# Optimization experiments

Measured on AMD Instinct MI355X. Metric: run time of the kernel, lower is better.

The kernel has to match this reference:

```python
import jax, jax.numpy as jnp
import numpy as np
import math

VOCAB = 256
EMBED = 1024
HEADS = 16
MAX_SEQ = 1024
B, S = 4, 1024
EPS = 1e-5


def setup_inputs() -> dict:
    key = jax.random.key(0)
    ks = jax.random.split(key, 10)
    x = jax.random.randint(ks[0], (B, S), 0, VOCAB)
    token_embedding = jax.random.normal(ks[1], (VOCAB, EMBED), dtype=jnp.float32)
    # positional phase buffer: pos * (1/10000**(dim/E)) * pi
    pos = jnp.arange(MAX_SEQ, dtype=jnp.float32)[:, None]
    dim = jnp.arange(EMBED, dtype=jnp.float32)[None, :]
    freq = 1.0 / (10000.0 ** (dim / EMBED))
    pos_phase = pos * freq * math.pi  # [MAX_SEQ, EMBED]
    hd = EMBED // HEADS
    q_rot = jax.random.uniform(ks[2], (HEADS, hd), minval=-math.pi, maxval=math.pi)
    k_rot = jax.random.uniform(ks[3], (HEADS, hd), minval=-math.pi, maxval=math.pi)
    v_rot = jax.random.uniform(ks[4], (HEADS, hd), minval=-math.pi, maxval=math.pi)
    # orthogonal-ish init for ff_real via QR
    a = jax.random.normal(ks[5], (EMBED, EMBED), dtype=jnp.float32)
    ff_real, _ = jnp.linalg.qr(a)
    ff_imag = jax.random.uniform(ks[6], (EMBED, EMBED), minval=-0.01, maxval=0.01)
    lim = 1.0 / math.sqrt(EMBED)
    ro_real_w = jax.random.uniform(ks[7], (VOCAB, EMBED), minval=-lim, maxval=lim)
    ro_real_b = jnp.zeros((VOCAB,), dtype=jnp.float32)
    ro_imag_w = jax.random.uniform(ks[8], (VOCAB, EMBED), minval=-lim, maxval=lim)
    ro_imag_b = jnp.zeros((VOCAB,), dtype=jnp.float32)
    return {
        "x": x,
        "token_embedding": token_embedding,
        "pos_phase": pos_phase,
        "q_rot": q_rot,
        "k_rot": k_rot,
        "v_rot": v_rot,
        "ff_real": ff_real,
        "ff_imag": ff_imag,
        "ro_real_w": ro_real_w,
        "ro_real_b": ro_real_b,
        "ro_imag_w": ro_imag_w,
        "ro_imag_b": ro_imag_b,
    }


def complex_norm(z):
    mag = jnp.abs(z)
    mean_mag = jnp.mean(mag, axis=-1, keepdims=True)
    std_mag = jnp.std(mag, axis=-1, keepdims=True, ddof=1)  # torch std is unbiased
    norm_mag = (mag - mean_mag) / (std_mag + EPS)
    scale = jnp.tanh(norm_mag) / (mag + EPS)
    return z * scale.astype(jnp.complex64)


def reference(x, token_embedding, pos_phase, q_rot, k_rot, v_rot,
              ff_real, ff_imag, ro_real_w, ro_real_b, ro_imag_w, ro_imag_b):
    b, s = x.shape
    h, hd = q_rot.shape
    mag = jnp.tanh(token_embedding[x])                       # [B,S,E]
    state = mag.astype(jnp.complex64) * jnp.exp(1j * pos_phase[:s].astype(jnp.complex64))[None]
    sh = state.reshape(b, s, h, hd)                          # [B,S,H,hd]
    q = sh * jnp.exp(1j * q_rot.astype(jnp.complex64))
    k = sh * jnp.exp(1j * k_rot.astype(jnp.complex64))
    v = sh * jnp.exp(1j * v_rot.astype(jnp.complex64))
    # complex QK^H interference -> take real part as logits
    interference = jnp.einsum('bqhd,bkhd->bhqk', q, jnp.conj(k))
    attn_logits = interference.real / math.sqrt(hd)
    causal = jnp.tril(jnp.ones((s, s), dtype=bool))
    attn_logits = jnp.where(causal[None, None], attn_logits, -jnp.inf)
    attn_weights = jax.nn.softmax(attn_logits * 8.0, axis=-1)  # [B,H,S,S]
    attn_out = jnp.einsum('bhqk,bkhd->bqhd', attn_weights.astype(jnp.complex64), v)
    attn_out = attn_out.reshape(b, s, h * hd)
    state = state + attn_out
    ff = ff_real.astype(jnp.complex64) + 1j * ff_imag.astype(jnp.complex64)
    state = state @ ff
    state = complex_norm(state)
    return state.real @ ro_real_w.T + ro_real_b + state.imag @ ro_imag_w.T + ro_imag_b
```

## Files before the change

kernel.cpp:

```cpp
#include <hip/hip_runtime.h>
#include <math.h>

#define B_ 4
#define S_ 1024
#define E_ 1024
#define H_ 16
#define V_ 256

typedef _Float16 h8 __attribute__((ext_vector_type(8)));
typedef _Float16 h4 __attribute__((ext_vector_type(4)));
typedef __fp16 f16x2 __attribute__((ext_vector_type(2)));
typedef int i2 __attribute__((ext_vector_type(2)));
typedef float f4x __attribute__((ext_vector_type(4)));

__device__ __forceinline__ void gload16(const void* g, void* l) {
  __builtin_amdgcn_global_load_lds((const __attribute__((address_space(1))) void*)g,
                                   (__attribute__((address_space(3))) void*)l, 16, 0, 0);
}

#define MFMA32F16(a, b, c) __builtin_amdgcn_mfma_f32_16x16x32_f16(a, b, c, 0, 0, 0)

#if defined(__has_builtin)
#if __has_builtin(__builtin_amdgcn_mfma_f32_16x16x16f16)
#define MFMA16F16(a, b, c) __builtin_amdgcn_mfma_f32_16x16x16f16(a, b, c, 0, 0, 0)
#endif
#endif
#ifndef MFMA16F16
__device__ __forceinline__ f4x mfma16f16_asm(h4 a, h4 b, f4x c) {
  asm volatile("v_mfma_f32_16x16x16_f16 %0, %1, %2, %0" : "+v"(c) : "v"(a), "v"(b));
  return c;
}
#define MFMA16F16(a, b, c) mfma16f16_asm(a, b, c)
#endif

__device__ __forceinline__ void fast_sincos(float x, float* s, float* c) {
  float rev = x * 0.15915494309189535f;
  rev = rev - floorf(rev);
  float sv, cv;
  asm("v_sin_f32 %0, %1" : "=v"(sv) : "v"(rev));
  asm("v_cos_f32 %0, %1" : "=v"(cv) : "v"(rev));
  *s = sv; *c = cv;
}
__device__ __forceinline__ float fast_tanh(float x) {
  return 1.0f - 2.0f / (__expf(2.0f * x) + 1.0f);
}
__device__ __forceinline__ float fast_exp2(float x) {
  float r;
  asm("v_exp_f32 %0, %1" : "=v"(r) : "v"(x));
  return r;
}

__global__ void rot_kernel(const float* __restrict__ qr, const float* __restrict__ kr,
                           const float* __restrict__ vr, float* __restrict__ tabs) {
  int i = blockIdx.x * blockDim.x + threadIdx.x;
  if (i >= 3 * 1024) return;
  int which = i >> 10;
  int j = i & 1023;
  const float* src = which == 0 ? qr : (which == 1 ? kr : vr);
  float s, c;
  sincosf(src[j], &s, &c);
  tabs[which * 2048 + j] = c;
  tabs[which * 2048 + 1024 + j] = s;
}

__global__ __launch_bounds__(256) void embed_qkv_kernel(
    const int* __restrict__ x, const float* __restrict__ te,
    const float* __restrict__ pp, const float* __restrict__ tabs,
    unsigned short* __restrict__ srh, unsigned short* __restrict__ sih,
    unsigned short* __restrict__ Kd, unsigned short* __restrict__ Vd) {
  __shared__ unsigned short Kl2[4096];
  __shared__ unsigned short Vl2[4096];
  const int kt2 = blockIdx.x;
  const int bh = blockIdx.y;
  const int b = bh >> 4, h = bh & 15;
  const int tid = threadIdx.x;
  const float* qc = tabs + h * 64;
  const float* qs = tabs + 1024 + h * 64;
  const float* kc = tabs + 2048 + h * 64;
  const float* ks = tabs + 3072 + h * 64;
  #pragma unroll
  for (int p = 0; p < 8; ++p) {
    int id = p * 256 + tid;
    int sl = id >> 6;
    int dd = id & 63;
    int s = kt2 * 32 + sl;
    int e = h * 64 + dd;
    int tok = x[b * 1024 + s];
    float mm = fast_tanh(te[tok * 1024 + e]);
    float sn, cs;
    fast_sincos(pp[s * 1024 + e], &sn, &cs);
    float re = mm * cs, im = mm * sn;
    size_t g = ((size_t)(b * 1024 + s)) * 1024 + e;
    *(_Float16*)&srh[g] = (_Float16)re;
    *(_Float16*)&sih[g] = (_Float16)im;
    float cq = qc[dd], sq = qs[dd], ck = kc[dd], sk = ks[dd];
    float cd = cq * ck + sq * sk;
    float sd = sq * ck - cq * sk;
    float kr = re * cd + im * sd;
    float ki = im * cd - re * sd;
    int t = sl >> 4, key = sl & 15;
    int c0 = dd, c1 = 64 + dd;
    #define KOFF(c) (t * 2048 + ((((c) >> 5) * 4 + (((c) >> 3) & 3)) * 16 + key) * 8 + ((c) & 7))
    *(_Float16*)&Kl2[KOFF(c0)] = (_Float16)kr;
    *(_Float16*)&Kl2[KOFF(c1)] = (_Float16)ki;
    #undef KOFF
    int kgk = key >> 2, jk = key & 3;
    #define VOFF(d) (t * 2048 + ((((d) >> 4) * 4 + kgk) * 16 + ((d) & 15)) * 4 + jk)
    *(_Float16*)&Vl2[VOFF(dd)] = (_Float16)re;
    *(_Float16*)&Vl2[VOFF(64 + dd)] = (_Float16)im;
    #undef VOFF
  }
  __syncthreads();
  unsigned short* kdst = Kd + ((size_t)(bh * 64 + kt2 * 2)) * 2048;
  unsigned short* vdst = Vd + ((size_t)(bh * 64 + kt2 * 2)) * 2048;
  #pragma unroll
  for (int p = 0; p < 2; ++p) {
    int c = p * 256 + tid;
    ((int4*)kdst)[c] = ((const int4*)Kl2)[c];
    ((int4*)vdst)[c] = ((const int4*)Vl2)[c];
  }
}

__global__ __launch_bounds__(256, 4) void attn_mfma_kernel(
    const unsigned short* __restrict__ srh, const unsigned short* __restrict__ sih,
    const unsigned short* __restrict__ Kd, const unsigned short* __restrict__ Vd,
    const float* __restrict__ tabs,
    unsigned short* __restrict__ Af) {
  __shared__ __align__(16) unsigned short Klds[2][4096];
  __shared__ __align__(16) unsigned short Vlds[2][4096];
  const int flat = blockIdx.x;
  const int low = flat & 7, rest = flat >> 3;
  const int a = rest >> 3;
  const int bh = ((rest & 7) << 3) | low;
  const int b = bh >> 4, h = bh & 15;
  const int tid = threadIdx.x, lane = tid & 63, wid = tid >> 6;
  const int cl = lane & 15, kg = lane >> 4;
  const int atile = (wid >> 1) ? (31 - a) : a;
  const int qw0 = atile * 32 + (wid & 1) * 16;

  h8 qf[4];
  {
    int q = qw0 + cl;
    const unsigned short* srow = srh + ((size_t)(b * 1024 + q)) * 1024 + h * 64;
    const unsigned short* irow = sih + ((size_t)(b * 1024 + q)) * 1024 + h * 64;
    #pragma unroll
    for (int ksx = 0; ksx < 4; ++ksx) {
      int f0 = ksx * 32 + kg * 8;
      qf[ksx] = (f0 < 64) ? *(const h8*)(srow + f0) : *(const h8*)(irow + (f0 - 64));
      qf[ksx] *= (_Float16)1.4426950408889634f;
    }
  }

  f4x acc[8] = {};
  float m_ = -1e30f, l_ = 0.f;
  const int np = 32 - a;
  const int wqmax = qw0 + 15;
  const int qcol = qw0 + cl;

  const unsigned short* kstream = Kd + ((size_t)(bh * 64)) * 2048;
  const unsigned short* vstream = Vd + ((size_t)(bh * 64)) * 2048;

  #define STAGE_PAIR(buf, P)                                                    \
    {                                                                           \
      const unsigned short* kb = kstream + (size_t)(P) * 4096;                  \
      const unsigned short* vb = vstream + (size_t)(P) * 4096;                  \
      _Pragma("unroll")                                                         \
      for (int r = 0; r < 2; ++r) {                                             \
        int off = r * 256 + wid * 64;                                           \
        gload16(kb + (size_t)(off + lane) * 8, &Klds[buf][off * 8]);            \
        gload16(vb + (size_t)(off + lane) * 8, &Vlds[buf][off * 8]);            \
      }                                                                         \
    }

  STAGE_PAIR(0, 0)
  __syncthreads();

  for (int p = 0; p < np; ++p) {
    const int cur = p & 1;
    if (p + 1 < np) STAGE_PAIR(cur ^ 1, p + 1)
    const int k0a = p * 32;
    if (k0a <= wqmax) {
      __builtin_amdgcn_s_setprio(1);
      f4x sca = {}, scb = {};
      #pragma unroll
      for (int ksx = 0; ksx < 4; ++ksx) {
        h8 ka = *(const h8*)&Klds[cur][ksx * 512 + lane * 8];
        sca = MFMA32F16(ka, qf[ksx], sca);
      }
      #pragma unroll
      for (int ksx = 0; ksx < 4; ++ksx) {
        h8 kb = *(const h8*)&Klds[cur][2048 + ksx * 512 + lane * 8];
        scb = MFMA32F16(kb, qf[ksx], scb);
      }
      __builtin_amdgcn_s_setprio(0);
      if (k0a + 31 > qw0) {
        #pragma unroll
        for (int r = 0; r < 4; ++r) {
          if (k0a + kg * 4 + r > qcol)      sca[r] = -1e30f;
          if (k0a + 16 + kg * 4 + r > qcol) scb[r] = -1e30f;
        }
      }
      float mA = fmaxf(fmaxf(sca[0], sca[1]), sca[2]);
      float mB = fmaxf(fmaxf(sca[3], scb[0]), scb[1]);
      float mC = fmaxf(fmaxf(scb[2], scb[3]), mA);
      float mx = fmaxf(mB, mC);
      mx = fmaxf(mx, __shfl_xor(mx, 16, 64));
      mx = fmaxf(mx, __shfl_xor(mx, 32, 64));
      if (!__all(mx <= m_ + 11.5416f)) {
        float mn = fmaxf(m_, mx);
        float corr = fast_exp2(m_ - mn);
        #pragma unroll
        for (int mt = 0; mt < 8; ++mt) acc[mt] *= corr;
        l_ *= corr;
        m_ = mn;
      }
      float pa0 = fast_exp2(sca[0] - m_), pa1 = fast_exp2(sca[1] - m_);
      float pa2 = fast_exp2(sca[2] - m_), pa3 = fast_exp2(sca[3] - m_);
      float pb0 = fast_exp2(scb[0] - m_), pb1 = fast_exp2(scb[1] - m_);
      float pb2 = fast_exp2(scb[2] - m_), pb3 = fast_exp2(scb[3] - m_);
      l_ += ((pa0 + pa1) + (pa2 + pa3)) + ((pb0 + pb1) + (pb2 + pb3));
      f16x2 a01 = __builtin_amdgcn_cvt_pkrtz(pa0, pa1);
      f16x2 a23 = __builtin_amdgcn_cvt_pkrtz(pa2, pa3);
      f16x2 b01 = __builtin_amdgcn_cvt_pkrtz(pb0, pb1);
      f16x2 b23 = __builtin_amdgcn_cvt_pkrtz(pb2, pb3);
      i2 ta, tb;
      ta[0] = __builtin_bit_cast(int, a01); ta[1] = __builtin_bit_cast(int, a23);
      tb[0] = __builtin_bit_cast(int, b01); tb[1] = __builtin_bit_cast(int, b23);
      h4 pba = __builtin_bit_cast(h4, ta);
      h4 pbb = __builtin_bit_cast(h4, tb);
      __builtin_amdgcn_s_setprio(1);
      #pragma unroll
      for (int mt = 0; mt < 8; ++mt) {
        h4 va = *(const h4*)&Vlds[cur][mt * 256 + lane * 4];
        acc[mt] = MFMA16F16(va, pba, acc[mt]);
      }
      #pragma unroll
      for (int mt = 0; mt < 8; ++mt) {
        h4 vb = *(const h4*)&Vlds[cur][2048 + mt * 256 + lane * 4];
        acc[mt] = MFMA16F16(vb, pbb, acc[mt]);
      }
      __builtin_amdgcn_s_setprio(0);
    }
    __syncthreads();
  }
  #undef STAGE_PAIR
  {
    l_ += __shfl_xor(l_, 16, 64);
    l_ += __shfl_xor(l_, 32, 64);
    float linv = 1.0f / l_;
    int q = qw0 + cl;
    size_t mrow = (size_t)(b * 1024 + q);
    size_t obase = mrow * 1024 + h * 64;
    size_t abase = mrow * 2048 + h * 64;
    #pragma unroll
    for (int mt = 0; mt < 4; ++mt) {
      int d0 = mt * 16 + kg * 4;
      h4 s_r = *(const h4*)&srh[obase + d0];
      h4 s_i = *(const h4*)&sih[obase + d0];
      h4 hr, hi;
      #pragma unroll
      for (int r = 0; r < 4; ++r) {
        int d = d0 + r;
        float orv = acc[mt][r] * linv;
        float oiv = acc[mt + 4][r] * linv;
        float c = tabs[4096 + h * 64 + d], s = tabs[5120 + h * 64 + d];
        hr[r] = (_Float16)(orv * c - oiv * s + (float)s_r[r]);
        hi[r] = (_Float16)(orv * s + oiv * c + (float)s_i[r]);
      }
      *(h4*)&Af[abase + d0]        = hr;
      *(h4*)&Af[abase + 1024 + d0] = hi;
    }
  }
}

__global__ void split_b_kernel(const float* __restrict__ fr, const float* __restrict__ fi,
                               unsigned short* __restrict__ Bt) {
  __shared__ float tile[32][33];
  const int k0 = blockIdx.x * 32, n0 = blockIdx.y * 32;
  const int tid = threadIdx.x;
  #pragma unroll
  for (int p = 0; p < 4; ++p) {
    int e = p * 256 + tid;
    int kk = e >> 5, nn = e & 31;
    int k = k0 + kk, n = n0 + nn;
    float v;
    if (n < 1024) v = (k < 1024) ? fr[(size_t)k * 1024 + n] : -fi[(size_t)(k - 1024) * 1024 + n];
    else          v = (k < 1024) ? fi[(size_t)k * 1024 + (n - 1024)]
                                 : fr[(size_t)(k - 1024) * 1024 + (n - 1024)];
    tile[kk][nn] = v;
  }
  __syncthreads();
  #pragma unroll
  for (int p = 0; p < 4; ++p) {
    int e = p * 256 + tid;
    int nn = e >> 5, kk = e & 31;
    *(_Float16*)&Bt[(size_t)(n0 + nn) * 2048 + (k0 + kk)] = (_Float16)tile[kk][nn];
  }
}

__global__ void split_w_kernel(const float* __restrict__ wr, const float* __restrict__ wi,
                               unsigned short* __restrict__ Wt) {
  int idx = blockIdx.x * 256 + threadIdx.x;
  int v = idx >> 9;
  int k4 = (idx & 511) * 4;
  float4 a = (k4 < 1024) ? *(const float4*)&wr[(size_t)v * 1024 + k4]
                         : *(const float4*)&wi[(size_t)v * 1024 + k4 - 1024];
  h4 h;
  h[0] = (_Float16)a.x; h[1] = (_Float16)a.y;
  h[2] = (_Float16)a.z; h[3] = (_Float16)a.w;
  *(h4*)&Wt[(size_t)v * 2048 + k4] = h;
}

__global__ __launch_bounds__(256, 4) void gemm_ff(
    const unsigned short* __restrict__ A,
    const unsigned short* __restrict__ Bt,
    float* __restrict__ pr0, float* __restrict__ pi0,
    float* __restrict__ pr1, float* __restrict__ pi1) {
  __shared__ short As[128 * 64];
  __shared__ short Bs[128 * 64];
  const int tid = threadIdx.x;
  const int lane = tid & 63, wid = tid >> 6;
  const int l = blockIdx.x + (blockIdx.y << 5);
  const int xcd = l & 7, j = l >> 3;
  const int m0 = ((xcd << 2) + (j & 3)) << 7;
  const int n0 = (j >> 2) << 7;
  const int z = blockIdx.z;
  const int wr = wid >> 1, wc = wid & 1;
  const int cl = lane & 15, rg = lane >> 4;

  f4x acc[4][4] = {};
  const int cbase = wid * 256;

  for (int kt = z * 16; kt < z * 16 + 16; ++kt) {
    const int k0 = kt * 64;
    #pragma unroll
    for (int it = 0; it < 4; ++it) {
      int c = cbase + it * 64 + lane;
      gload16(A + (size_t)(m0 + (c >> 3)) * 2048 + k0 + (c & 7) * 8,
              As + (cbase + it * 64) * 8);
      gload16(Bt + (size_t)(n0 + (c >> 3)) * 2048 + k0 + (c & 7) * 8,
              Bs + (cbase + it * 64) * 8);
    }
    __syncthreads();
    #pragma unroll
    for (int ks = 0; ks < 2; ++ks) {
      h8 a[4], b[4];
      #pragma unroll
      for (int ms = 0; ms < 4; ++ms)
        a[ms] = *(const h8*)&As[(wr * 64 + ms * 16 + cl) * 64 + ks * 32 + rg * 8];
      #pragma unroll
      for (int ns = 0; ns < 4; ++ns)
        b[ns] = *(const h8*)&Bs[(wc * 64 + ns * 16 + cl) * 64 + ks * 32 + rg * 8];
      #pragma unroll
      for (int ms = 0; ms < 4; ++ms)
        #pragma unroll
        for (int ns = 0; ns < 4; ++ns)
          acc[ms][ns] = MFMA32F16(a[ms], b[ns], acc[ms][ns]);
    }
    __syncthreads();
  }

  const int colbase = n0 + wc * 64;
  float* o_r = z ? pr1 : pr0;
  float* o_i = z ? pi1 : pi0;
  float* dst = (colbase < 1024) ? o_r : o_i;
  const int cb = colbase & 1023;
  #pragma unroll
  for (int ms = 0; ms < 4; ++ms)
    #pragma unroll
    for (int r2 = 0; r2 < 4; ++r2) {
      const int grow = m0 + wr * 64 + ms * 16 + rg * 4 + r2;
      #pragma unroll
      for (int ns = 0; ns < 4; ++ns)
        dst[(size_t)grow * 1024 + cb + ns * 16 + cl] = acc[ms][ns][r2];
    }
}

__global__ __launch_bounds__(256, 4) void gemm_ro(
    const unsigned short* __restrict__ Z,
    const unsigned short* __restrict__ Wt,
    float* __restrict__ part) {
  __shared__ short As[128 * 64];
  __shared__ short Bs[128 * 64];
  const int tid = threadIdx.x;
  const int lane = tid & 63, wid = tid >> 6;
  const int l = blockIdx.x + (blockIdx.y << 5);
  const int xcd = l & 7, j = l >> 3;
  const int m0 = ((xcd << 2) + (j & 3)) << 7;
  const int n0 = (j >> 2) << 7;
  const int z = blockIdx.z;
  const int wr = wid >> 1, wc = wid & 1;
  const int cl = lane & 15, rg = lane >> 4;

  f4x acc[4][4] = {};
  const int cbase = wid * 256;

  for (int kt = z * 8; kt < z * 8 + 8; ++kt) {
    const int k0 = kt * 64;
    #pragma unroll
    for (int it = 0; it < 4; ++it) {
      int c = cbase + it * 64 + lane;
      gload16(Z + (size_t)(m0 + (c >> 3)) * 2048 + k0 + (c & 7) * 8,
              As + (cbase + it * 64) * 8);
      gload16(Wt + (size_t)(n0 + (c >> 3)) * 2048 + k0 + (c & 7) * 8,
              Bs + (cbase + it * 64) * 8);
    }
    __syncthreads();
    #pragma unroll
    for (int ks = 0; ks < 2; ++ks) {
      h8 a[4], b[4];
      #pragma unroll
      for (int ms = 0; ms < 4; ++ms)
        a[ms] = *(const h8*)&As[(wr * 64 + ms * 16 + cl) * 64 + ks * 32 + rg * 8];
      #pragma unroll
      for (int ns = 0; ns < 4; ++ns)
        b[ns] = *(const h8*)&Bs[(wc * 64 + ns * 16 + cl) * 64 + ks * 32 + rg * 8];
      #pragma unroll
      for (int ms = 0; ms < 4; ++ms)
        #pragma unroll
        for (int ns = 0; ns < 4; ++ns)
          acc[ms][ns] = MFMA32F16(a[ms], b[ns], acc[ms][ns]);
    }
    __syncthreads();
  }

  float* dst = part + (size_t)z * 4096 * 256;
  const int colbase = n0 + wc * 64;
  #pragma unroll
  for (int ms = 0; ms < 4; ++ms)
    #pragma unroll
    for (int r2 = 0; r2 < 4; ++r2) {
      const int grow = m0 + wr * 64 + ms * 16 + rg * 4 + r2;
      #pragma unroll
      for (int ns = 0; ns < 4; ++ns)
        dst[(size_t)grow * 256 + colbase + ns * 16 + cl] = acc[ms][ns][r2];
    }
}

__global__ __launch_bounds__(256) void norm_split_kernel(
    const float* __restrict__ pr0, const float* __restrict__ pi0,
    const float* __restrict__ pr1, const float* __restrict__ pi1,
    unsigned short* __restrict__ Z) {
  const int row = blockIdx.x, tid = threadIdx.x;
  const int base = row * E_ + tid * 4;
  float4 r0 = *(const float4*)&pr0[base];
  float4 r1 = *(const float4*)&pr1[base];
  float4 i0 = *(const float4*)&pi0[base];
  float4 i1 = *(const float4*)&pi1[base];
  float4 zr = make_float4(r0.x + r1.x, r0.y + r1.y, r0.z + r1.z, r0.w + r1.w);
  float4 zi = make_float4(i0.x + i1.x, i0.y + i1.y, i0.z + i1.z, i0.w + i1.w);
  float mg[4];
  mg[0] = sqrtf(zr.x * zr.x + zi.x * zi.x);
  mg[1] = sqrtf(zr.y * zr.y + zi.y * zi.y);
  mg[2] = sqrtf(zr.z * zr.z + zi.z * zi.z);
  mg[3] = sqrtf(zr.w * zr.w + zi.w * zi.w);
  float s1 = mg[0] + mg[1] + mg[2] + mg[3];
  float s2 = mg[0]*mg[0] + mg[1]*mg[1] + mg[2]*mg[2] + mg[3]*mg[3];
  #pragma unroll
  for (int off = 1; off < 64; off <<= 1) {
    s1 += __shfl_xor(s1, off, 64);
    s2 += __shfl_xor(s2, off, 64);
  }
  __shared__ float ws1[4], ws2[4];
  if ((tid & 63) == 0) { ws1[tid >> 6] = s1; ws2[tid >> 6] = s2; }
  __syncthreads();
  s1 = ws1[0] + ws1[1] + ws1[2] + ws1[3];
  s2 = ws2[0] + ws2[1] + ws2[2] + ws2[3];
  float mean = s1 * (1.0f / 1024.0f);
  float var = (s2 - 1024.0f * mean * mean) * (1.0f / 1023.0f);
  var = fmaxf(var, 0.0f);
  float inv_sd = 1.0f / (sqrtf(var) + 1e-5f);
  float sc[4];
  #pragma unroll
  for (int t = 0; t < 4; ++t)
    sc[t] = tanhf((mg[t] - mean) * inv_sd) / (mg[t] + 1e-5f);
  h4 hr, hi;
  hr[0] = (_Float16)(zr.x * sc[0]); hr[1] = (_Float16)(zr.y * sc[1]);
  hr[2] = (_Float16)(zr.z * sc[2]); hr[3] = (_Float16)(zr.w * sc[3]);
  hi[0] = (_Float16)(zi.x * sc[0]); hi[1] = (_Float16)(zi.y * sc[1]);
  hi[2] = (_Float16)(zi.z * sc[2]); hi[3] = (_Float16)(zi.w * sc[3]);
  const size_t zb = (size_t)row * 2048 + tid * 4;
  *(h4*)&Z[zb]        = hr;
  *(h4*)&Z[zb + 1024] = hi;
}

__global__ void reduce_bias_kernel(const float* __restrict__ part,
                                   const float* __restrict__ rb,
                                   const float* __restrict__ ib,
                                   float* __restrict__ out) {
  int i4 = (blockIdx.x * 256 + threadIdx.x) * 4;
  int col = i4 & 255;
  float4 s = *(const float4*)&part[i4];
  #pragma unroll
  for (int z = 1; z < 4; ++z) {
    float4 v = *(const float4*)&part[(size_t)z * 1048576 + i4];
    s.x += v.x; s.y += v.y; s.z += v.z; s.w += v.w;
  }
  s.x += rb[col + 0] + ib[col + 0];
  s.y += rb[col + 1] + ib[col + 1];
  s.z += rb[col + 2] + ib[col + 2];
  s.w += rb[col + 3] + ib[col + 3];
  *(float4*)&out[i4] = s;
}

extern "C" void kernel_launch(void* const* d_in, const int* in_sizes, int n_in,
                              void* d_out, int out_size, void* d_ws, size_t ws_size,
                              hipStream_t stream) {
  const int*   x    = (const int*)d_in[0];
  const float* te   = (const float*)d_in[1];
  const float* pp   = (const float*)d_in[2];
  const float* qr   = (const float*)d_in[3];
  const float* kr   = (const float*)d_in[4];
  const float* vr   = (const float*)d_in[5];
  const float* ffr  = (const float*)d_in[6];
  const float* ffi  = (const float*)d_in[7];
  const float* rorw = (const float*)d_in[8];
  const float* rorb = (const float*)d_in[9];
  const float* roiw = (const float*)d_in[10];
  const float* roib = (const float*)d_in[11];
  float* out = (float*)d_out;

  char* W = (char*)d_ws;
  const size_t MiB = 1 << 20;
  unsigned short* srh = (unsigned short*)W;
  unsigned short* sih = (unsigned short*)(W + 16 * MiB);
  unsigned short* Af = (unsigned short*)(W + 32 * MiB);
  unsigned short* Kd = (unsigned short*)(W + 48 * MiB);
  unsigned short* Vd = (unsigned short*)(W + 64 * MiB);
  unsigned short* Bt = (unsigned short*)(W + 48 * MiB);
  unsigned short* Wt = (unsigned short*)(W + 56 * MiB);
  float* tabs = (float*)(W + 96 * MiB);
  float* pr0 = (float*)W;
  float* pi0 = (float*)(W + 16 * MiB);
  float* pr1 = (float*)(W + 64 * MiB);
  float* pi1 = (float*)(W + 80 * MiB);
  unsigned short* Zhl = Af;
  float* ro_part = (float*)(W + 64 * MiB);

  rot_kernel<<<12, 256, 0, stream>>>(qr, kr, vr, tabs);
  embed_qkv_kernel<<<dim3(32, 64), 256, 0, stream>>>(x, te, pp, tabs, srh, sih, Kd, Vd);
  attn_mfma_kernel<<<1024, 256, 0, stream>>>(srh, sih, Kd, Vd, tabs, Af);
  split_b_kernel<<<dim3(64, 64), 256, 0, stream>>>(ffr, ffi, Bt);
  split_w_kernel<<<512, 256, 0, stream>>>(rorw, roiw, Wt);
  gemm_ff<<<dim3(32, 16, 2), 256, 0, stream>>>(Af, Bt, pr0, pi0, pr1, pi1);
  norm_split_kernel<<<B_ * S_, 256, 0, stream>>>(pr0, pi0, pr1, pi1, Zhl);
  gemm_ro<<<dim3(32, 2, 4), 256, 0, stream>>>(Zhl, Wt, ro_part);
  reduce_bias_kernel<<<1024, 256, 0, stream>>>(ro_part, rorb, roib, out);
}
```

Measured before the change: 145.9 us.

## Double-buffer LDS tiles in feed-forward and readout GEMMs

Both MFMA GEMM kernels now keep two LDS stages for the A and B tiles. The first two K-tiles are prefetched up front, and the load for tile t+2 is issued right after the barrier that ends compute on tile t. This lets global-to-LDS copies overlap the MFMA work on the next tile instead of serialising load, barrier and compute. In exchange LDS per block doubles and launch bounds drop from 4 to 2 blocks per CU, so there is less latency hiding from occupancy.

```diff
diff --git a/kernel.cpp b/kernel.cpp
--- a/kernel.cpp
+++ b/kernel.cpp
@@ -311,13 +311,13 @@
   *(h4*)&Wt[(size_t)v * 2048 + k4] = h;
 }
 
-__global__ __launch_bounds__(256, 4) void gemm_ff(
+__global__ __launch_bounds__(256, 2) void gemm_ff(
     const unsigned short* __restrict__ A,
     const unsigned short* __restrict__ Bt,
     float* __restrict__ pr0, float* __restrict__ pi0,
     float* __restrict__ pr1, float* __restrict__ pi1) {
-  __shared__ short As[128 * 64];
-  __shared__ short Bs[128 * 64];
+  __shared__ short As[2][128 * 64];
+  __shared__ short Bs[2][128 * 64];
   const int tid = threadIdx.x;
   const int lane = tid & 63, wid = tid >> 6;
   const int l = blockIdx.x + (blockIdx.y << 5);
@@ -327,30 +327,39 @@
   const int z = blockIdx.z;
   const int wr = wid >> 1, wc = wid & 1;
   const int cl = lane & 15, rg = lane >> 4;
+  const int cbase = wid * 256;
 
   f4x acc[4][4] = {};
-  const int cbase = wid * 256;
-
-  for (int kt = z * 16; kt < z * 16 + 16; ++kt) {
-    const int k0 = kt * 64;
-    #pragma unroll
-    for (int it = 0; it < 4; ++it) {
-      int c = cbase + it * 64 + lane;
-      gload16(A + (size_t)(m0 + (c >> 3)) * 2048 + k0 + (c & 7) * 8,
-              As + (cbase + it * 64) * 8);
-      gload16(Bt + (size_t)(n0 + (c >> 3)) * 2048 + k0 + (c & 7) * 8,
-              Bs + (cbase + it * 64) * 8);
-    }
-    __syncthreads();
+
+  #define FF_STAGE(bf, kt)                                                      \
+    {                                                                           \
+      const int k0s = (kt) * 64;                                                \
+      _Pragma("unroll")                                                         \
+      for (int it = 0; it < 4; ++it) {                                          \
+        int c = cbase + it * 64 + lane;                                         \
+        gload16(A + (size_t)(m0 + (c >> 3)) * 2048 + k0s + (c & 7) * 8,         \
+                As[bf] + (cbase + it * 64) * 8);                                \
+        gload16(Bt + (size_t)(n0 + (c >> 3)) * 2048 + k0s + (c & 7) * 8,        \
+                Bs[bf] + (cbase + it * 64) * 8);                                \
+      }                                                                         \
+    }
+
+  const int ktbase = z * 16;
+  FF_STAGE(0, ktbase)
+  FF_STAGE(1, ktbase + 1)
+  __syncthreads();
+
+  for (int t = 0; t < 16; ++t) {
+    const int bf = t & 1;
     #pragma unroll
     for (int ks = 0; ks < 2; ++ks) {
       h8 a[4], b[4];
       #pragma unroll
       for (int ms = 0; ms < 4; ++ms)
-        a[ms] = *(const h8*)&As[(wr * 64 + ms * 16 + cl) * 64 + ks * 32 + rg * 8];
+        a[ms] = *(const h8*)&As[bf][(wr * 64 + ms * 16 + cl) * 64 + ks * 32 + rg * 8];
       #pragma unroll
       for (int ns = 0; ns < 4; ++ns)
-        b[ns] = *(const h8*)&Bs[(wc * 64 + ns * 16 + cl) * 64 + ks * 32 + rg * 8];
+        b[ns] = *(const h8*)&Bs[bf][(wc * 64 + ns * 16 + cl) * 64 + ks * 32 + rg * 8];
       #pragma unroll
       for (int ms = 0; ms < 4; ++ms)
         #pragma unroll
@@ -358,7 +367,9 @@
           acc[ms][ns] = MFMA32F16(a[ms], b[ns], acc[ms][ns]);
     }
     __syncthreads();
-  }
+    if (t + 2 < 16) FF_STAGE(bf, ktbase + t + 2)
+  }
+  #undef FF_STAGE
 
   const int colbase = n0 + wc * 64;
   float* o_r = z ? pr1 : pr0;
@@ -376,12 +387,12 @@
     }
 }
 
-__global__ __launch_bounds__(256, 4) void gemm_ro(
+__global__ __launch_bounds__(256, 2) void gemm_ro(
     const unsigned short* __restrict__ Z,
     const unsigned short* __restrict__ Wt,
     float* __restrict__ part) {
-  __shared__ short As[128 * 64];
-  __shared__ short Bs[128 * 64];
+  __shared__ short As[2][128 * 64];
+  __shared__ short Bs[2][128 * 64];
   const int tid = threadIdx.x;
   const int lane = tid & 63, wid = tid >> 6;
   const int l = blockIdx.x + (blockIdx.y << 5);
@@ -391,30 +402,39 @@
   const int z = blockIdx.z;
   const int wr = wid >> 1, wc = wid & 1;
   const int cl = lane & 15, rg = lane >> 4;
+  const int cbase = wid * 256;
 
   f4x acc[4][4] = {};
-  const int cbase = wid * 256;
-
-  for (int kt = z * 8; kt < z * 8 + 8; ++kt) {
-    const int k0 = kt * 64;
-    #pragma unroll
-    for (int it = 0; it < 4; ++it) {
-      int c = cbase + it * 64 + lane;
-      gload16(Z + (size_t)(m0 + (c >> 3)) * 2048 + k0 + (c & 7) * 8,
-              As + (cbase + it * 64) * 8);
-      gload16(Wt + (size_t)(n0 + (c >> 3)) * 2048 + k0 + (c & 7) * 8,
-              Bs + (cbase + it * 64) * 8);
-    }
-    __syncthreads();
+
+  #define RO_STAGE(bf, kt)                                                      \
+    {                                                                           \
+      const int k0s = (kt) * 64;                                                \
+      _Pragma("unroll")                                                         \
+      for (int it = 0; it < 4; ++it) {                                          \
+        int c = cbase + it * 64 + lane;                                         \
+        gload16(Z + (size_t)(m0 + (c >> 3)) * 2048 + k0s + (c & 7) * 8,         \
+                As[bf] + (cbase + it * 64) * 8);                                \
+        gload16(Wt + (size_t)(n0 + (c >> 3)) * 2048 + k0s + (c & 7) * 8,        \
+                Bs[bf] + (cbase + it * 64) * 8);                                \
+      }                                                                         \
+    }
+
+  const int ktbase = z * 8;
+  RO_STAGE(0, ktbase)
+  RO_STAGE(1, ktbase + 1)
+  __syncthreads();
+
+  for (int t = 0; t < 8; ++t) {
+    const int bf = t & 1;
     #pragma unroll
     for (int ks = 0; ks < 2; ++ks) {
       h8 a[4], b[4];
       #pragma unroll
       for (int ms = 0; ms < 4; ++ms)
-        a[ms] = *(const h8*)&As[(wr * 64 + ms * 16 + cl) * 64 + ks * 32 + rg * 8];
+        a[ms] = *(const h8*)&As[bf][(wr * 64 + ms * 16 + cl) * 64 + ks * 32 + rg * 8];
       #pragma unroll
       for (int ns = 0; ns < 4; ++ns)
-        b[ns] = *(const h8*)&Bs[(wc * 64 + ns * 16 + cl) * 64 + ks * 32 + rg * 8];
+        b[ns] = *(const h8*)&Bs[bf][(wc * 64 + ns * 16 + cl) * 64 + ks * 32 + rg * 8];
       #pragma unroll
       for (int ms = 0; ms < 4; ++ms)
         #pragma unroll
@@ -422,7 +442,9 @@
           acc[ms][ns] = MFMA32F16(a[ms], b[ns], acc[ms][ns]);
     }
     __syncthreads();
-  }
+    if (t + 2 < 8) RO_STAGE(bf, ktbase + t + 2)
+  }
+  #undef RO_STAGE
 
   float* dst = part + (size_t)z * 4096 * 256;
   const int colbase = n0 + wc * 64;
```

Measured after the change: 156.5 us. +7.2%, slower.

## Double-buffer LDS tiles in gemm_ff with a K-step of 32

Applied to the files above, without the earlier changes.

The single 128x64 LDS tile per operand in gemm_ff becomes two 128x32 buffers. Loads for step t+2 are issued right after the barrier that ends compute on step t, so global-to-LDS transfers overlap with MFMA work on the other buffer. Total LDS use stays the same, but the K-step is halved, so there are twice as many barriers per block. Any overlap also depends on how the barrier's waitcnt handling interacts with the in-flight global_load_lds.

```diff
diff --git a/kernel.cpp b/kernel.cpp
--- a/kernel.cpp
+++ b/kernel.cpp
@@ -316,8 +316,8 @@
     const unsigned short* __restrict__ Bt,
     float* __restrict__ pr0, float* __restrict__ pi0,
     float* __restrict__ pr1, float* __restrict__ pi1) {
-  __shared__ short As[128 * 64];
-  __shared__ short Bs[128 * 64];
+  __shared__ short As[2][128 * 32];
+  __shared__ short Bs[2][128 * 32];
   const int tid = threadIdx.x;
   const int lane = tid & 63, wid = tid >> 6;
   const int l = blockIdx.x + (blockIdx.y << 5);
@@ -327,38 +327,46 @@
   const int z = blockIdx.z;
   const int wr = wid >> 1, wc = wid & 1;
   const int cl = lane & 15, rg = lane >> 4;
+  const int cb2 = wid * 128;
 
   f4x acc[4][4] = {};
-  const int cbase = wid * 256;
-
-  for (int kt = z * 16; kt < z * 16 + 16; ++kt) {
-    const int k0 = kt * 64;
-    #pragma unroll
-    for (int it = 0; it < 4; ++it) {
-      int c = cbase + it * 64 + lane;
-      gload16(A + (size_t)(m0 + (c >> 3)) * 2048 + k0 + (c & 7) * 8,
-              As + (cbase + it * 64) * 8);
-      gload16(Bt + (size_t)(n0 + (c >> 3)) * 2048 + k0 + (c & 7) * 8,
-              Bs + (cbase + it * 64) * 8);
-    }
+
+  #define FF_STAGE(bf, kt)                                                      \
+    {                                                                           \
+      const int k0s = (kt) * 32;                                                \
+      _Pragma("unroll")                                                         \
+      for (int it = 0; it < 2; ++it) {                                          \
+        int c = cb2 + it * 64 + lane;                                           \
+        gload16(A + (size_t)(m0 + (c >> 2)) * 2048 + k0s + (c & 3) * 8,         \
+                As[bf] + (cb2 + it * 64) * 8);                                  \
+        gload16(Bt + (size_t)(n0 + (c >> 2)) * 2048 + k0s + (c & 3) * 8,        \
+                Bs[bf] + (cb2 + it * 64) * 8);                                  \
+      }                                                                         \
+    }
+
+  const int ktbase = z * 32;
+  FF_STAGE(0, ktbase)
+  FF_STAGE(1, ktbase + 1)
+  __syncthreads();
+
+  for (int t = 0; t < 32; ++t) {
+    const int bf = t & 1;
+    h8 a[4], b[4];
+    #pragma unroll
+    for (int ms = 0; ms < 4; ++ms)
+      a[ms] = *(const h8*)&As[bf][(wr * 64 + ms * 16 + cl) * 32 + rg * 8];
+    #pragma unroll
+    for (int ns = 0; ns < 4; ++ns)
+      b[ns] = *(const h8*)&Bs[bf][(wc * 64 + ns * 16 + cl) * 32 + rg * 8];
+    #pragma unroll
+    for (int ms = 0; ms < 4; ++ms)
+      #pragma unroll
+      for (int ns = 0; ns < 4; ++ns)
+        acc[ms][ns] = MFMA32F16(a[ms], b[ns], acc[ms][ns]);
     __syncthreads();
-    #pragma unroll
-    for (int ks = 0; ks < 2; ++ks) {
-      h8 a[4], b[4];
-      #pragma unroll
-      for (int ms = 0; ms < 4; ++ms)
-        a[ms] = *(const h8*)&As[(wr * 64 + ms * 16 + cl) * 64 + ks * 32 + rg * 8];
-      #pragma unroll
-      for (int ns = 0; ns < 4; ++ns)
-        b[ns] = *(const h8*)&Bs[(wc * 64 + ns * 16 + cl) * 64 + ks * 32 + rg * 8];
-      #pragma unroll
-      for (int ms = 0; ms < 4; ++ms)
-        #pragma unroll
-        for (int ns = 0; ns < 4; ++ns)
-          acc[ms][ns] = MFMA32F16(a[ms], b[ns], acc[ms][ns]);
-    }
-    __syncthreads();
-  }
+    if (t + 2 < 32) FF_STAGE(bf, ktbase + t + 2)
+  }
+  #undef FF_STAGE
 
   const int colbase = n0 + wc * 64;
   float* o_r = z ? pr1 : pr0;
```

Result: no change. 146.7 us (+0.5%).
